# Performance work log

Measured on AMD Instinct MI355X. Metric: run time of the kernel, lower is better.

The kernel has to match this reference:

```python
import jax, jax.numpy as jnp
import numpy as np

NN_SIZE = 16  # nn_size from __init__


def _knn_idx(points_ref, k):
    """Brute-force KNN of points_ref against itself (replaces faiss_knn).
    Returns (B, N, k) neighbor indices, self point excluded."""
    sq = jnp.sum(points_ref * points_ref, axis=-1)  # (B, N)
    # squared pairwise distances (B, N, N)
    d2 = sq[:, :, None] + sq[:, None, :] - 2.0 * jnp.einsum(
        'bnd,bmd->bnm', points_ref, points_ref)
    _, idx = jax.lax.top_k(-d2, k + 1)  # nearest first; idx[...,0] is self
    return idx[:, :, 1:]


def _edge_lengths(pts, knn_idx):
    """Gather neighbor coords and compute edge lengths (B, N, K)."""
    group = jax.vmap(lambda p, i: p[i])(pts, knn_idx)  # (B, N, K, D)
    return jnp.linalg.norm(group - pts[:, :, None, :], axis=-1)


def setup_inputs() -> dict:
    key = jax.random.key(0)
    k1, k2 = jax.random.split(key)
    B, N, D = 4, 8192, 3
    points_ref = jax.random.normal(k1, (B, N, D), dtype=jnp.float32)
    # pred points: perturbed ref so the loss is non-degenerate
    points = points_ref + 0.01 * jax.random.normal(k2, (B, N, D), dtype=jnp.float32)
    return {"points_ref": points_ref, "points": points}


def reference(points_ref, points):
    # faiss KNN is non-differentiable -> stop_gradient on the index search
    knn_idx = _knn_idx(jax.lax.stop_gradient(points_ref), NN_SIZE)  # (B,N,K)
    dist_ref = _edge_lengths(points_ref, knn_idx)  # (B, N, K)
    dist = _edge_lengths(points, knn_idx)          # (B, N, K)
    # metric = torch.nn.L1Loss() (mean reduction)
    return jnp.mean(jnp.abs(dist_ref - dist))
```

## Files before the change

### kernel.cpp

```cpp
#include <hip/hip_runtime.h>
#include <math.h>

#define BATCH 4
#define NPTS  8192
#define KNN   16
#define KK    17
#define QPB   16
#define SPLITS 16
#define BLOCK (QPB*SPLITS)
#define RANGE (NPTS/SPLITS)
#define SAMPLE 64
#define AL    8
#define CAP   21
#define CHUNK 4
#define NQ    (BATCH*NPTS)
#define GRIDQ (NQ/QPB)
#define JMASK 0x1FFFu
#define EMASK 0xFFFFE000u
#define TOTAL_EDGES (BATCH*NPTS*KNN)

__global__ void pel_pack(const float* __restrict__ pref, const float* __restrict__ pts,
                         float4* __restrict__ p4r, float4* __restrict__ p4p,
                         float* __restrict__ acc, unsigned* __restrict__ bcnt) {
    const int idx = blockIdx.x * 256 + threadIdx.x;
    if (idx == 0) { acc[0] = 0.0f; bcnt[0] = 0u; }
    if (idx < NQ) {
        float x = pref[3*idx], y = pref[3*idx+1], z = pref[3*idx+2];
        p4r[idx] = make_float4(-2.f*x, -2.f*y, -2.f*z, fmaf(x, x, fmaf(y, y, z*z)));
        x = pts[3*idx]; y = pts[3*idx+1]; z = pts[3*idx+2];
        p4p[idx] = make_float4(-2.f*x, -2.f*y, -2.f*z, fmaf(x, x, fmaf(y, y, z*z)));
    }
}

__device__ __forceinline__ unsigned mkkey(const float4 p, float xi, float yi,
                                          float zi, float sqi, unsigned j) {
    const float e  = fmaf(p.x, xi, fmaf(p.y, yi, p.z * zi)) + p.w;
    const float d2 = e + sqi;
    return (__float_as_uint(d2) & EMASK) | j;
}

__device__ __forceinline__ void ins17(unsigned (&a)[KK], unsigned key) {
    #pragma unroll
    for (int k = KK - 1; k >= 1; --k) a[k] = min(a[k], max(a[k - 1], key));
    a[0] = min(a[0], key);
}

template<int RL>
__device__ __forceinline__ unsigned merge_tau(const unsigned (*s_key)[BLOCK], int t) {
    const int mq = t & (QPB - 1), half = (t >> 4) & 1;
    unsigned m[KK];
    #pragma unroll
    for (int k = 0; k < KK; ++k) m[k] = 0xFFFFFFFFu;
    for (int s = 8 * half; s < 8 * half + 8; ++s) {
        const int col = mq + s * QPB;
        for (int k = 0; k < RL; ++k) {
            const unsigned c = s_key[k][col];
            if (c >= m[KK - 1]) break;
            ins17(m, c);
        }
    }
    unsigned tau = 0;
    #pragma unroll
    for (int k = 0; k < KK; ++k) {
        const unsigned bk = (unsigned)__shfl_xor((int)m[KK - 1 - k], 16, 64);
        tau = max(tau, min(m[k], bk));
    }
    return tau;
}

__global__ __launch_bounds__(BLOCK, 8)
void pel_main(const float4* __restrict__ P4r, const float4* __restrict__ P4p,
              float* __restrict__ acc_ws, unsigned* __restrict__ bcnt,
              float* __restrict__ out)
{
    __shared__ unsigned s_key[CAP][BLOCK];
    __shared__ unsigned s_tau[QPB];
    __shared__ float s_part[BLOCK / 64];

    const int t  = threadIdx.x;
    const int lq = t & (QPB - 1);
    const int sp = t >> 4;
    const int q  = blockIdx.x * QPB + lq;
    const int b  = q >> 13;
    const int i  = q & (NPTS - 1);

    const float4* __restrict__ Pq = P4r + b * NPTS;
    const float4* __restrict__ Pp = P4p + b * NPTS;

    const float4 self = Pq[i];
    const float xi = -0.5f * self.x, yi = -0.5f * self.y, zi = -0.5f * self.z;
    const float sqi = self.w;
    const unsigned base = (unsigned)(sp * RANGE);
    const float4* __restrict__ Pb = Pq + base;

    unsigned al[AL];
    #pragma unroll
    for (int k = 0; k < AL; ++k) al[k] = 0xFFFFFFFFu;
    for (int j0 = 0; j0 < SAMPLE; j0 += CHUNK) {
        float4 c[CHUNK];
        #pragma unroll
        for (int u = 0; u < CHUNK; ++u) c[u] = Pb[j0 + u];
        #pragma unroll
        for (int u = 0; u < CHUNK; ++u) {
            const unsigned key = mkkey(c[u], xi, yi, zi, sqi, base + j0 + u);
            #pragma unroll
            for (int k = AL - 1; k >= 1; --k) al[k] = min(al[k], max(al[k - 1], key));
            al[0] = min(al[0], key);
        }
    }
    #pragma unroll
    for (int k = 0; k < AL; ++k) s_key[k][t] = al[k];
    __syncthreads();
    {
        const unsigned tau0 = merge_tau<AL>(s_key, t);
        if (t < QPB) s_tau[t] = tau0;
    }
    __syncthreads();
    unsigned tauL = s_tau[lq];

    int cnt = 0;
    for (int j0 = 0; j0 < RANGE; j0 += CHUNK) {
        float4 c[CHUNK];
        #pragma unroll
        for (int u = 0; u < CHUNK; ++u) c[u] = Pb[j0 + u];
        #pragma unroll
        for (int u = 0; u < CHUNK; ++u) {
            const unsigned key = mkkey(c[u], xi, yi, zi, sqi, base + j0 + u);
            s_key[cnt][t] = key;
            cnt += (key <= tauL) ? 1 : 0;
        }
        if (cnt > CAP - CHUNK) {
            unsigned k17[KK];
            #pragma unroll
            for (int k = 0; k < KK; ++k) k17[k] = 0xFFFFFFFFu;
            for (int n = 0; n < cnt; ++n) ins17(k17, s_key[n][t]);
            const unsigned th = k17[KK - 1];
            int kept = 0;
            for (int n = 0; n < cnt; ++n) {
                const unsigned c2 = s_key[n][t];
                if (c2 <= th) { s_key[kept][t] = c2; ++kept; }
            }
            cnt = kept;
            tauL = min(tauL, th);
        }
    }

    unsigned c17[KK];
    #pragma unroll
    for (int k = 0; k < KK; ++k) c17[k] = 0xFFFFFFFFu;
    for (int n = 0; n < cnt; ++n) ins17(c17, s_key[n][t]);
    __syncthreads();
    #pragma unroll
    for (int k = 0; k < KK; ++k) s_key[k][t] = c17[k];
    __syncthreads();
    {
        const unsigned tauX = merge_tau<KK>(s_key, t);
        if (t < QPB) s_tau[t] = tauX;
    }
    __syncthreads();
    const unsigned tauK = s_tau[lq];

    const float4 selfp = Pp[i];
    const float pxi = -0.5f * selfp.x, pyi = -0.5f * selfp.y, pzi = -0.5f * selfp.z;
    float accv = 0.0f;
    #pragma unroll
    for (int k = 0; k < KK; ++k) {
        if (c17[k] <= tauK) {
            const int j = (int)(c17[k] & JMASK);
            const float4 pr = Pq[j];
            const float er  = fmaf(pr.x, xi, fmaf(pr.y, yi, pr.z * zi)) + pr.w;
            const float d2r = fmaxf(er + sqi, 0.0f);
            const float4 pp = Pp[j];
            const float ep  = fmaf(pp.x, pxi, fmaf(pp.y, pyi, pp.z * pzi)) + pp.w;
            const float d2p = fmaxf(ep + selfp.w, 0.0f);
            accv += fabsf(sqrtf(d2r) - sqrtf(d2p));
        }
    }

    #pragma unroll
    for (int o = 32; o > 0; o >>= 1) accv += __shfl_down(accv, o, 64);
    if ((t & 63) == 0) s_part[t >> 6] = accv;
    __syncthreads();
    if (t == 0) {
        float s = 0.0f;
        #pragma unroll
        for (int w = 0; w < BLOCK / 64; ++w) s += s_part[w];
        atomicAdd(acc_ws, s);
        __threadfence();
        const unsigned old = atomicAdd(bcnt, 1u);
        if (old == GRIDQ - 1) {
            __threadfence();
            const float total = atomicAdd(acc_ws, 0.0f);
            out[0] = total * (1.0f / (float)TOTAL_EDGES);
        }
    }
}

extern "C" void kernel_launch(void* const* d_in, const int* in_sizes, int n_in,
                              void* d_out, int out_size, void* d_ws, size_t ws_size,
                              hipStream_t stream) {
    const float* pref = (const float*)d_in[0];
    const float* pts  = (const float*)d_in[1];
    float*    acc  = (float*)d_ws;
    unsigned* bcnt = (unsigned*)d_ws + 1;
    float4*   P4r  = (float4*)((char*)d_ws + 16);
    float4*   P4p  = P4r + NQ;
    float*    out  = (float*)d_out;

    pel_pack<<<NQ / 256, 256, 0, stream>>>(pref, pts, P4r, P4p, acc, bcnt);
    pel_main<<<GRIDQ, BLOCK, 0, stream>>>(P4r, P4p, acc, bcnt, out);
}
```

Before: 290.9 us.

## Morton-sort points into grid cells and prefilter KNN candidates by block bounding sphere

Adds histogram, scan and scatter kernels that bin reference points into a 32^3 grid and reorder them in Morton order, so the 16 queries in a block are spatially close. Each block seeds its neighbour threshold from a small window of nearby sorted points. It then builds a bounding sphere around its queries and culls all 8192 points with one dot-product test per point. Only surviving candidates are compacted via ballot into shared memory and get the per-query distance and top-17 selection. This removes most per-query distance work, at the cost of three extra launches, a memset, atomics in the scatter, and more synchronisation in the query loop.

```diff
diff --git a/kernel.cpp b/kernel.cpp
--- a/kernel.cpp
+++ b/kernel.cpp
@@ -5,46 +5,53 @@
 #define NPTS  8192
 #define KNN   16
 #define KK    17
-#define QPB   16
-#define SPLITS 16
-#define BLOCK (QPB*SPLITS)
-#define RANGE (NPTS/SPLITS)
-#define SAMPLE 64
-#define AL    8
-#define CAP   21
-#define CHUNK 4
 #define NQ    (BATCH*NPTS)
-#define GRIDQ (NQ/QPB)
 #define JMASK 0x1FFFu
 #define EMASK 0xFFFFE000u
 #define TOTAL_EDGES (BATCH*NPTS*KNN)
 
-__global__ void pel_pack(const float* __restrict__ pref, const float* __restrict__ pts,
-                         float4* __restrict__ p4r, float4* __restrict__ p4p,
-                         float* __restrict__ acc, unsigned* __restrict__ bcnt) {
-    const int idx = blockIdx.x * 256 + threadIdx.x;
-    if (idx == 0) { acc[0] = 0.0f; bcnt[0] = 0u; }
-    if (idx < NQ) {
-        float x = pref[3*idx], y = pref[3*idx+1], z = pref[3*idx+2];
-        p4r[idx] = make_float4(-2.f*x, -2.f*y, -2.f*z, fmaf(x, x, fmaf(y, y, z*z)));
-        x = pts[3*idx]; y = pts[3*idx+1]; z = pts[3*idx+2];
-        p4p[idx] = make_float4(-2.f*x, -2.f*y, -2.f*z, fmaf(x, x, fmaf(y, y, z*z)));
-    }
-}
-
+#define GC    32
+#define GLO   (-4.5f)
+#define GINV  (32.0f/9.0f)
+#define NCELL (GC*GC*GC)
+
+#define QPB   16
+#define BLOCK 256
+#define GRIDQ (NQ/QPB)
+#define WIN   64
+#define SEGCAP 512
+#define CAP   21
+
+__device__ __forceinline__ int cell_coord(float x) {
+    int c = (int)floorf((x - GLO) * GINV);
+    return min(GC - 1, max(0, c));
+}
+__device__ __forceinline__ unsigned spread5(unsigned v) {
+    v &= 31u;
+    v = (v | (v << 8)) & 0x100Fu;
+    v = (v | (v << 4)) & 0x10C3u;
+    v = (v | (v << 2)) & 0x1249u;
+    return v;
+}
+__device__ __forceinline__ unsigned morton_id(float x, float y, float z) {
+    return spread5((unsigned)cell_coord(x)) | (spread5((unsigned)cell_coord(y)) << 1)
+         | (spread5((unsigned)cell_coord(z)) << 2);
+}
 __device__ __forceinline__ unsigned mkkey(const float4 p, float xi, float yi,
                                           float zi, float sqi, unsigned j) {
     const float e  = fmaf(p.x, xi, fmaf(p.y, yi, p.z * zi)) + p.w;
     const float d2 = e + sqi;
     return (__float_as_uint(d2) & EMASK) | j;
 }
-
 __device__ __forceinline__ void ins17(unsigned (&a)[KK], unsigned key) {
     #pragma unroll
     for (int k = KK - 1; k >= 1; --k) a[k] = min(a[k], max(a[k - 1], key));
     a[0] = min(a[0], key);
 }
-
+__device__ __forceinline__ unsigned mbcnt64(unsigned long long m) {
+    return __builtin_amdgcn_mbcnt_hi((unsigned)(m >> 32),
+           __builtin_amdgcn_mbcnt_lo((unsigned)m, 0u));
+}
 template<int RL>
 __device__ __forceinline__ unsigned merge_tau(const unsigned (*s_key)[BLOCK], int t) {
     const int mq = t & (QPB - 1), half = (t >> 4) & 1;
@@ -68,18 +75,64 @@
     return tau;
 }
 
-__global__ __launch_bounds__(BLOCK, 8)
-void pel_main(const float4* __restrict__ P4r, const float4* __restrict__ P4p,
-              float* __restrict__ acc_ws, unsigned* __restrict__ bcnt,
-              float* __restrict__ out)
+__global__ void pel_hist(const float* __restrict__ pref, unsigned* __restrict__ hist,
+                         float* __restrict__ acc, unsigned* __restrict__ bcnt) {
+    const int idx = blockIdx.x * 256 + threadIdx.x;
+    if (idx == 0) { acc[0] = 0.0f; bcnt[0] = 0u; }
+    const int b = idx >> 13;
+    const unsigned mid = morton_id(pref[3*idx], pref[3*idx+1], pref[3*idx+2]);
+    atomicAdd(&hist[b * NCELL + mid], 1u);
+}
+__global__ __launch_bounds__(1024)
+void pel_scan(const unsigned* __restrict__ hist, unsigned* __restrict__ off) {
+    __shared__ unsigned s[1024];
+    const unsigned* h = hist + blockIdx.x * NCELL;
+    unsigned*       o = off  + blockIdx.x * NCELL;
+    const int t = threadIdx.x;
+    unsigned v[32], tot = 0;
+    #pragma unroll
+    for (int k = 0; k < 32; ++k) { v[k] = h[t * 32 + k]; tot += v[k]; }
+    s[t] = tot;
+    __syncthreads();
+    for (int d = 1; d < 1024; d <<= 1) {
+        const unsigned add = (t >= d) ? s[t - d] : 0u;
+        __syncthreads();
+        s[t] += add;
+        __syncthreads();
+    }
+    unsigned run = s[t] - tot;
+    #pragma unroll
+    for (int k = 0; k < 32; ++k) { o[t * 32 + k] = run; run += v[k]; }
+}
+__global__ void pel_scatter(const float* __restrict__ pref, const float* __restrict__ pts,
+                            unsigned* __restrict__ off,
+                            float4* __restrict__ p4r, float4* __restrict__ p4p) {
+    const int idx = blockIdx.x * 256 + threadIdx.x;
+    const int b = idx >> 13;
+    const float x = pref[3*idx], y = pref[3*idx+1], z = pref[3*idx+2];
+    const unsigned mid = morton_id(x, y, z);
+    const unsigned pos = atomicAdd(&off[b * NCELL + mid], 1u);
+    p4r[b * NPTS + pos] = make_float4(-2.f*x, -2.f*y, -2.f*z, fmaf(x, x, fmaf(y, y, z*z)));
+    const float px = pts[3*idx], py = pts[3*idx+1], pz = pts[3*idx+2];
+    p4p[b * NPTS + pos] = make_float4(-2.f*px, -2.f*py, -2.f*pz,
+                                      fmaf(px, px, fmaf(py, py, pz*pz)));
+}
+
+__global__ __launch_bounds__(BLOCK, 6)
+void pel_query(const float4* __restrict__ P4r, const float4* __restrict__ P4p,
+               float* __restrict__ acc_ws, unsigned* __restrict__ bcnt,
+               float* __restrict__ out)
 {
     __shared__ unsigned s_key[CAP][BLOCK];
+    __shared__ unsigned short s_seg[4][SEGCAP];
     __shared__ unsigned s_tau[QPB];
+    __shared__ float s_grp[4];
+    __shared__ int s_cnt[4], s_done[4];
     __shared__ float s_part[BLOCK / 64];
 
     const int t  = threadIdx.x;
-    const int lq = t & (QPB - 1);
-    const int sp = t >> 4;
+    const int lq = t & (QPB - 1), sp = t >> 4;
+    const int wv = t >> 6, lane = t & 63;
     const int q  = blockIdx.x * QPB + lq;
     const int b  = q >> 13;
     const int i  = q & (NPTS - 1);
@@ -90,70 +143,114 @@
     const float4 self = Pq[i];
     const float xi = -0.5f * self.x, yi = -0.5f * self.y, zi = -0.5f * self.z;
     const float sqi = self.w;
-    const unsigned base = (unsigned)(sp * RANGE);
-    const float4* __restrict__ Pb = Pq + base;
-
-    unsigned al[AL];
-    #pragma unroll
-    for (int k = 0; k < AL; ++k) al[k] = 0xFFFFFFFFu;
-    for (int j0 = 0; j0 < SAMPLE; j0 += CHUNK) {
-        float4 c[CHUNK];
-        #pragma unroll
-        for (int u = 0; u < CHUNK; ++u) c[u] = Pb[j0 + u];
-        #pragma unroll
-        for (int u = 0; u < CHUNK; ++u) {
-            const unsigned key = mkkey(c[u], xi, yi, zi, sqi, base + j0 + u);
+
+    unsigned al[4] = {~0u, ~0u, ~0u, ~0u};
+    const int w0 = min(max(i - WIN / 2, 0), NPTS - WIN) + sp * 4;
+    {
+        float4 cw[4];
+        #pragma unroll
+        for (int u = 0; u < 4; ++u) cw[u] = Pq[w0 + u];
+        #pragma unroll
+        for (int u = 0; u < 4; ++u) {
+            const unsigned key = mkkey(cw[u], xi, yi, zi, sqi, (unsigned)(w0 + u));
             #pragma unroll
-            for (int k = AL - 1; k >= 1; --k) al[k] = min(al[k], max(al[k - 1], key));
+            for (int k = 3; k >= 1; --k) al[k] = min(al[k], max(al[k - 1], key));
             al[0] = min(al[0], key);
         }
     }
     #pragma unroll
-    for (int k = 0; k < AL; ++k) s_key[k][t] = al[k];
-    __syncthreads();
-    {
-        const unsigned tau0 = merge_tau<AL>(s_key, t);
+    for (int k = 0; k < 4; ++k) s_key[k][t] = al[k];
+    __syncthreads();
+    if (t < 32) {
+        const unsigned tau0 = merge_tau<4>(s_key, t);
         if (t < QPB) s_tau[t] = tau0;
     }
     __syncthreads();
+
+    if (t < QPB) {
+        const int i2 = (blockIdx.x * QPB + t) & (NPTS - 1);
+        const float4 s2 = Pq[i2];
+        const float qx = -0.5f * s2.x, qy = -0.5f * s2.y, qz = -0.5f * s2.z;
+        float mnx = qx, mxx = qx, mny = qy, mxy = qy, mnz = qz, mxz = qz;
+        #pragma unroll
+        for (int m = 1; m <= 8; m <<= 1) {
+            mnx = fminf(mnx, __shfl_xor(mnx, m, 64)); mxx = fmaxf(mxx, __shfl_xor(mxx, m, 64));
+            mny = fminf(mny, __shfl_xor(mny, m, 64)); mxy = fmaxf(mxy, __shfl_xor(mxy, m, 64));
+            mnz = fminf(mnz, __shfl_xor(mnz, m, 64)); mxz = fmaxf(mxz, __shfl_xor(mxz, m, 64));
+        }
+        const float cx = 0.5f * (mnx + mxx), cy = 0.5f * (mny + mxy), cz = 0.5f * (mnz + mxz);
+        const float dq = sqrtf((qx-cx)*(qx-cx) + (qy-cy)*(qy-cy) + (qz-cz)*(qz-cz));
+        const float rt = sqrtf(__uint_as_float((s_tau[t] & EMASK) + 0x2000u));
+        float v = dq + rt;
+        #pragma unroll
+        for (int m = 1; m <= 8; m <<= 1) v = fmaxf(v, __shfl_xor(v, m, 64));
+        if (t == 0) {
+            const float R = v + 1e-3f;
+            s_grp[0] = R * R - (cx*cx + cy*cy + cz*cz);
+            s_grp[1] = cx; s_grp[2] = cy; s_grp[3] = cz;
+        }
+    }
+    __syncthreads();
+    const float thr = s_grp[0], gcx = s_grp[1], gcy = s_grp[2], gcz = s_grp[3];
+
     unsigned tauL = s_tau[lq];
-
-    int cnt = 0;
-    for (int j0 = 0; j0 < RANGE; j0 += CHUNK) {
-        float4 c[CHUNK];
-        #pragma unroll
-        for (int u = 0; u < CHUNK; ++u) c[u] = Pb[j0 + u];
-        #pragma unroll
-        for (int u = 0; u < CHUNK; ++u) {
-            const unsigned key = mkkey(c[u], xi, yi, zi, sqi, base + j0 + u);
-            s_key[cnt][t] = key;
-            cnt += (key <= tauL) ? 1 : 0;
-        }
-        if (cnt > CAP - CHUNK) {
-            unsigned k17[KK];
-            #pragma unroll
-            for (int k = 0; k < KK; ++k) k17[k] = 0xFFFFFFFFu;
-            for (int n = 0; n < cnt; ++n) ins17(k17, s_key[n][t]);
-            const unsigned th = k17[KK - 1];
-            int kept = 0;
-            for (int n = 0; n < cnt; ++n) {
-                const unsigned c2 = s_key[n][t];
-                if (c2 <= th) { s_key[kept][t] = c2; ++kept; }
+    int cnt2 = 0;
+    int kch = 0;
+    for (;;) {
+        __syncthreads();
+        int scnt = 0;
+        while (kch < 32 && scnt <= SEGCAP - 64) {
+            const int j = ((kch << 2) + wv) * 64 + lane;
+            const float4 p = Pq[j];
+            const float e = fmaf(p.x, gcx, fmaf(p.y, gcy, fmaf(p.z, gcz, p.w)));
+            const bool a = (e <= thr);
+            const unsigned long long mk = __ballot(a);
+            if (a) s_seg[wv][scnt + mbcnt64(mk)] = (unsigned short)j;
+            scnt += (int)__popcll(mk);
+            ++kch;
+        }
+        if (lane == 0) { s_cnt[wv] = scnt; s_done[wv] = (kch >= 32) ? 1 : 0; }
+        __syncthreads();
+        for (int w2 = 0; w2 < 4; ++w2) {
+            const int c = s_cnt[w2];
+            int n = sp;
+            unsigned jj0 = 0; float4 p0;
+            if (n < c) { jj0 = s_seg[w2][n]; p0 = Pq[jj0]; }
+            while (n < c) {
+                const int n2 = n + QPB;
+                unsigned jj1 = 0; float4 p1;
+                if (n2 < c) { jj1 = s_seg[w2][n2]; p1 = Pq[jj1]; }
+                const unsigned key = mkkey(p0, xi, yi, zi, sqi, jj0);
+                s_key[cnt2][t] = key;
+                cnt2 += (key <= tauL) ? 1 : 0;
+                if (cnt2 == CAP) {
+                    unsigned k17[KK];
+                    #pragma unroll
+                    for (int k = 0; k < KK; ++k) k17[k] = 0xFFFFFFFFu;
+                    for (int n3 = 0; n3 < cnt2; ++n3) ins17(k17, s_key[n3][t]);
+                    const unsigned th = k17[KK - 1];
+                    int kept = 0;
+                    for (int n3 = 0; n3 < cnt2; ++n3) {
+                        const unsigned c2 = s_key[n3][t];
+                        if (c2 <= th) { s_key[kept][t] = c2; ++kept; }
+                    }
+                    cnt2 = kept; tauL = min(tauL, th);
+                }
+                jj0 = jj1; p0 = p1; n = n2;
             }
-            cnt = kept;
-            tauL = min(tauL, th);
-        }
+        }
+        if (s_done[0] && s_done[1] && s_done[2] && s_done[3]) break;
     }
 
     unsigned c17[KK];
     #pragma unroll
     for (int k = 0; k < KK; ++k) c17[k] = 0xFFFFFFFFu;
-    for (int n = 0; n < cnt; ++n) ins17(c17, s_key[n][t]);
+    for (int n = 0; n < cnt2; ++n) ins17(c17, s_key[n][t]);
     __syncthreads();
     #pragma unroll
     for (int k = 0; k < KK; ++k) s_key[k][t] = c17[k];
     __syncthreads();
-    {
+    if (t < 32) {
         const unsigned tauX = merge_tau<KK>(s_key, t);
         if (t < QPB) s_tau[t] = tauX;
     }
@@ -179,12 +276,12 @@
 
     #pragma unroll
     for (int o = 32; o > 0; o >>= 1) accv += __shfl_down(accv, o, 64);
-    if ((t & 63) == 0) s_part[t >> 6] = accv;
+    if (lane == 0) s_part[wv] = accv;
     __syncthreads();
     if (t == 0) {
         float s = 0.0f;
         #pragma unroll
-        for (int w = 0; w < BLOCK / 64; ++w) s += s_part[w];
+        for (int w2 = 0; w2 < BLOCK / 64; ++w2) s += s_part[w2];
         atomicAdd(acc_ws, s);
         __threadfence();
         const unsigned old = atomicAdd(bcnt, 1u);
@@ -201,12 +298,17 @@
                               hipStream_t stream) {
     const float* pref = (const float*)d_in[0];
     const float* pts  = (const float*)d_in[1];
-    float*    acc  = (float*)d_ws;
-    unsigned* bcnt = (unsigned*)d_ws + 1;
-    float4*   P4r  = (float4*)((char*)d_ws + 16);
+    float4*   P4r  = (float4*)d_ws;
     float4*   P4p  = P4r + NQ;
+    unsigned* hist = (unsigned*)d_ws;
+    unsigned* off  = (unsigned*)((char*)d_ws + 1048576);
+    float*    acc  = (float*)((char*)d_ws + 1572864);
+    unsigned* bcnt = (unsigned*)(acc + 1);
     float*    out  = (float*)d_out;
 
-    pel_pack<<<NQ / 256, 256, 0, stream>>>(pref, pts, P4r, P4p, acc, bcnt);
-    pel_main<<<GRIDQ, BLOCK, 0, stream>>>(P4r, P4p, acc, bcnt, out);
-}
+    hipMemsetAsync(hist, 0, BATCH * NCELL * sizeof(unsigned), stream);
+    pel_hist   <<<NQ / 256, 256, 0, stream>>>(pref, hist, acc, bcnt);
+    pel_scan   <<<BATCH, 1024, 0, stream>>>(hist, off);
+    pel_scatter<<<NQ / 256, 256, 0, stream>>>(pref, pts, off, P4r, P4p);
+    pel_query  <<<GRIDQ, BLOCK, 0, stream>>>(P4r, P4p, acc, bcnt, out);
+}
```

Result: slower. 377.9 us (+29.9%).
